# Optimization experiments

Measured on AMD Instinct MI355X. Metric: run time of the kernel, lower is better.

Reference implementation:

```python
import jax, jax.numpy as jnp
import numpy as np

NUM_STEPS = 3
NUM_HEADS = 8
HEAD_DIM = 128
EPS = 1e-5


def layernorm(x, g, b):
    mu = jnp.mean(x, -1, keepdims=True)
    var = jnp.mean(jnp.square(x - mu), -1, keepdims=True)
    return (x - mu) * jax.lax.rsqrt(var + EPS) * g + b


def entmax15(x):
    # Exact entmax-1.5 along last axis (Peters & Martins 2019, sort-based).
    x = (x - jnp.max(x, -1, keepdims=True)) / 2.0
    xs = jnp.flip(jnp.sort(x, -1), -1)  # descending sort
    rho = jnp.arange(1, x.shape[-1] + 1, dtype=x.dtype)
    mean = jnp.cumsum(xs, -1) / rho
    meansq = jnp.cumsum(xs * xs, -1) / rho
    ss = rho * (meansq - jnp.square(mean))
    tau = mean - jnp.sqrt(jnp.clip((1.0 - ss) / rho, 0.0, None))
    support = jnp.sum(tau <= xs, -1, keepdims=True)
    tau_star = jnp.take_along_axis(tau, support - 1, -1)
    return jnp.square(jnp.clip(x - tau_star, 0.0, None))


def setup_inputs() -> dict:
    key = jax.random.key(0)
    ks = jax.random.split(key, 6)
    B, S, Hd, Md, N = 2, 1024, 2048, 1024, 2048
    THD = NUM_HEADS * HEAD_DIM
    return {
        "hidden": jax.random.normal(ks[0], (B, S, Hd), jnp.float32),
        "memory": jax.random.normal(ks[1], (N, Md), jnp.float32),
        "Wq": jax.random.normal(ks[2], (THD, Hd), jnp.float32) / np.float32(np.sqrt(Hd)),
        "Wk": jax.random.normal(ks[3], (THD, Md), jnp.float32) / np.float32(np.sqrt(Md)),
        "Wv": jax.random.normal(ks[4], (THD, Md), jnp.float32) / np.float32(np.sqrt(Md)),
        "Wo": jax.random.normal(ks[5], (Hd, THD), jnp.float32) / np.float32(np.sqrt(THD)),
        "log_beta": jnp.full((NUM_HEADS,), float(np.log(1.0 / np.sqrt(HEAD_DIM))), jnp.float32),
        "g_state": jnp.ones((Hd,), jnp.float32),
        "b_state": jnp.zeros((Hd,), jnp.float32),
        "g_mem": jnp.ones((Md,), jnp.float32),
        "b_mem": jnp.zeros((Md,), jnp.float32),
    }


def reference(hidden, memory, Wq, Wk, Wv, Wo, log_beta, g_state, b_state, g_mem, b_mem):
    B, S, _ = hidden.shape
    N = memory.shape[0]
    H, hd = NUM_HEADS, HEAD_DIM
    # projections
    Q = layernorm(hidden, g_state, b_state) @ Wq.T            # (B,S,H*hd)
    mn = layernorm(memory, g_mem, b_mem)                      # (N,Md)
    K = (mn @ Wk.T).reshape(N, H, hd).transpose(1, 0, 2)      # (H,N,hd)
    V = (mn @ Wv.T).reshape(N, H, hd).transpose(1, 0, 2)      # (H,N,hd)
    xi = Q.reshape(B, S, H, hd).transpose(0, 2, 1, 3)          # (B,H,S,hd)
    beta = jnp.exp(log_beta)[None, :, None, None]
    for _ in range(NUM_STEPS):
        scores = jnp.einsum('bhsd,hnd->bhsn', xi, K) * beta    # (B,H,S,N)
        w = entmax15(scores)
        xi = jnp.einsum('bhsn,hnd->bhsd', w, V)
    out = xi.transpose(0, 2, 1, 3).reshape(B, S, H * hd) @ Wo.T  # (B,S,hidden_dim)
    return out
```

## Files before the change

### kernel.cpp

```cpp
#include <hip/hip_runtime.h>

typedef _Float16 half8 __attribute__((ext_vector_type(8)));
typedef _Float16 hv4 __attribute__((ext_vector_type(4)));
typedef float fv4 __attribute__((ext_vector_type(4)));

typedef __attribute__((address_space(3))) unsigned lds_u32;
typedef const __attribute__((address_space(1))) unsigned glb_u32;

__device__ __forceinline__ void gll16(const void* g, void* l) {
  __builtin_amdgcn_global_load_lds((glb_u32*)g, (lds_u32*)l, 16, 0, 0);
}

__device__ __forceinline__ void ln_body(const float* __restrict__ in, const float* __restrict__ g,
                                        const float* __restrict__ bb, _Float16* __restrict__ out,
                                        int ncols, int row) {
  __shared__ float sm[8];
  int t = threadIdx.x;
  const float* rp = in + (size_t)row * ncols;
  int nv = ncols >> 10;
  fv4 v[2];
  float s1 = 0.f, s2 = 0.f;
#pragma unroll
  for (int c = 0; c < 2; ++c)
    if (c < nv) {
      v[c] = *(const fv4*)(rp + c * 1024 + t * 4);
#pragma unroll
      for (int j = 0; j < 4; ++j) { s1 += v[c][j]; s2 += v[c][j] * v[c][j]; }
    }
#pragma unroll
  for (int off = 32; off > 0; off >>= 1) { s1 += __shfl_xor(s1, off, 64); s2 += __shfl_xor(s2, off, 64); }
  int w = t >> 6;
  if ((t & 63) == 0) { sm[w] = s1; sm[4 + w] = s2; }
  __syncthreads();
  s1 = sm[0] + sm[1] + sm[2] + sm[3];
  s2 = sm[4] + sm[5] + sm[6] + sm[7];
  float inv = 1.0f / (float)ncols;
  float mu = s1 * inv;
  float var = s2 * inv - mu * mu;
  float rstd = rsqrtf(var + 1e-5f);
#pragma unroll
  for (int c = 0; c < 2; ++c)
    if (c < nv) {
      int col = c * 1024 + t * 4;
      fv4 gg = *(const fv4*)(g + col);
      fv4 bv = *(const fv4*)(bb + col);
      hv4 o;
#pragma unroll
      for (int j = 0; j < 4; ++j) o[j] = (_Float16)(((v[c][j] - mu) * rstd) * gg[j] + bv[j]);
      *(hv4*)(out + (size_t)row * ncols + col) = o;
    }
}

__global__ __launch_bounds__(256) void ln_all(const float* __restrict__ hid,
                                              const float* __restrict__ mem,
                                              const float* __restrict__ gs, const float* __restrict__ bs,
                                              const float* __restrict__ gm, const float* __restrict__ bm,
                                              _Float16* __restrict__ oh, _Float16* __restrict__ om) {
  int b = blockIdx.x;
  if (b < 2048) ln_body(hid, gs, bs, oh, 2048, b);
  else ln_body(mem, gm, bm, om, 1024, b - 2048);
}

__global__ __launch_bounds__(256) void cast_all(const float* __restrict__ s0, _Float16* __restrict__ d0,
                                                const float* __restrict__ s1, _Float16* __restrict__ d1,
                                                const float* __restrict__ s2, _Float16* __restrict__ d2,
                                                const float* __restrict__ s3, _Float16* __restrict__ d3) {
  int b = blockIdx.x;
  const float* s;
  _Float16* d;
  int off;
  if (b < 2048) { s = s0; d = d0; off = b; }
  else if (b < 3072) { s = s1; d = d1; off = b - 2048; }
  else if (b < 4096) { s = s2; d = d2; off = b - 3072; }
  else { s = s3; d = d3; off = b - 4096; }
  int i = (off * 256 + threadIdx.x) << 2;
  fv4 f = *(const fv4*)(s + i);
  hv4 h;
#pragma unroll
  for (int j = 0; j < 4; ++j) h[j] = (_Float16)f[j];
  *(hv4*)(d + i) = h;
}

__global__ __launch_bounds__(256) void reduce_split(const float* __restrict__ parts, int ns,
                                                    long long stride,
                                                    _Float16* __restrict__ hi, int n) {
  int i = (blockIdx.x * 256 + threadIdx.x) << 2;
  if (i < n) {
    fv4 s = *(const fv4*)(parts + i);
    for (int j = 1; j < ns; ++j) {
      fv4 v = *(const fv4*)(parts + (size_t)j * stride + i);
      s += v;
    }
    hv4 h;
#pragma unroll
    for (int j = 0; j < 4; ++j) h[j] = (_Float16)s[j];
    *(hv4*)(hi + i) = h;
  }
}

__global__ __launch_bounds__(256) void entmax_c(const _Float16* __restrict__ scores,
                                                float* __restrict__ crow) {
  __shared__ float comp[4][512];
  int wid = threadIdx.x >> 6;
  int row = blockIdx.x * 4 + wid;
  int l = threadIdx.x & 63;
  unsigned long long lmask = (1ull << l) - 1ull;
  const half8* sp = (const half8*)(scores + (size_t)row * 2048);
  half8 hx[4];
#pragma unroll
  for (int i = 0; i < 4; ++i) hx[i] = sp[i * 64 + l];
  fv4 x[8];
#pragma unroll
  for (int i = 0; i < 4; ++i)
#pragma unroll
    for (int j = 0; j < 8; ++j) x[i * 2 + (j >> 2)][j & 3] = (float)hx[i][j];
  float m = x[0][0];
#pragma unroll
  for (int i = 0; i < 8; ++i)
#pragma unroll
    for (int j = 0; j < 4; ++j) m = fmaxf(m, x[i][j]);
#pragma unroll
  for (int off = 32; off > 0; off >>= 1) m = fmaxf(m, __shfl_xor(m, off, 64));
#pragma unroll
  for (int i = 0; i < 8; ++i)
#pragma unroll
    for (int j = 0; j < 4; ++j) x[i][j] = (x[i][j] - m) * 0.5f;

  float tau = -1.0f;
  bool fixed = false;
  int cnti = 2048;
  for (int it = 0; it < 6 && !fixed; ++it) {
    float s1 = 0.f, s2 = 0.f;
    cnti = 0;
#pragma unroll
    for (int i = 0; i < 8; ++i)
#pragma unroll
      for (int j = 0; j < 4; ++j) {
        bool a = x[i][j] > tau;
        cnti += (int)__builtin_popcountll(__ballot(a));
        float sel = a ? x[i][j] : 0.f;
        s1 += sel;
        s2 = fmaf(sel, sel, s2);
      }
#pragma unroll
    for (int off = 32; off > 0; off >>= 1) {
      s1 += __shfl_xor(s1, off, 64);
      s2 += __shfl_xor(s2, off, 64);
    }
    float cnt = (float)cnti;
    float mean = s1 / cnt;
    float ss = s2 - s1 * mean;
    float nt = mean - sqrtf(fmaxf((1.0f - ss) / cnt, 0.0f));
    if (nt == tau) fixed = true;
    else tau = nt;
    if (cnti <= 512) break;
  }
  if (!fixed) {
    if (cnti <= 512) {
      int base = 0;
#pragma unroll
      for (int i = 0; i < 8; ++i)
#pragma unroll
        for (int j = 0; j < 4; ++j) {
          bool a = x[i][j] > tau;
          unsigned long long mk = __ballot(a);
          if (a) comp[wid][base + (int)__builtin_popcountll(mk & lmask)] = x[i][j];
          base += (int)__builtin_popcountll(mk);
        }
      float y[8];
#pragma unroll
      for (int r = 0; r < 8; ++r) {
        int idx = r * 64 + l;
        y[r] = (idx < base) ? comp[wid][idx] : -2.0f;
      }
      for (int it = 0; it < 10 && !fixed; ++it) {
        float s1 = 0.f, s2 = 0.f;
        int c = 0;
#pragma unroll
        for (int r = 0; r < 8; ++r) {
          bool a = y[r] > tau;
          c += (int)__builtin_popcountll(__ballot(a));
          float sel = a ? y[r] : 0.f;
          s1 += sel;
          s2 = fmaf(sel, sel, s2);
        }
#pragma unroll
        for (int off = 32; off > 0; off >>= 1) {
          s1 += __shfl_xor(s1, off, 64);
          s2 += __shfl_xor(s2, off, 64);
        }
        float cnt = (float)c;
        float mean = s1 / cnt;
        float ss = s2 - s1 * mean;
        float nt = mean - sqrtf(fmaxf((1.0f - ss) / cnt, 0.0f));
        if (nt == tau) fixed = true;
        else tau = nt;
      }
    } else {
      for (int it = 0; it < 8 && !fixed; ++it) {
        float s1 = 0.f, s2 = 0.f;
        int c = 0;
#pragma unroll
        for (int i = 0; i < 8; ++i)
#pragma unroll
          for (int j = 0; j < 4; ++j) {
            bool a = x[i][j] > tau;
            c += (int)__builtin_popcountll(__ballot(a));
            float sel = a ? x[i][j] : 0.f;
            s1 += sel;
            s2 = fmaf(sel, sel, s2);
          }
#pragma unroll
        for (int off = 32; off > 0; off >>= 1) {
          s1 += __shfl_xor(s1, off, 64);
          s2 += __shfl_xor(s2, off, 64);
        }
        float cnt = (float)c;
        float mean = s1 / cnt;
        float ss = s2 - s1 * mean;
        float nt = mean - sqrtf(fmaxf((1.0f - ss) / cnt, 0.0f));
        if (nt == tau) fixed = true;
        else tau = nt;
      }
    }
  }

  if (l == 0) crow[row] = 0.5f * m + tau;
}

struct GemmParams {
  const _Float16 *A, *B, *B2;
  const float* crow;
  _Float16 *C16, *C16b;
  float* C32;
  const float* log_beta;
  int K, lda, ldb;
  long long aSB, aSH, bSH;
  long long crowSB, crowSH;
  long long cSB, cSH, cOsR, cOsC;
  long long cOsRb, cOsCb;
  long long partStride;
  int alphaMode, outMode, outModeB, nsplit, dual;
  int gx, gy, swz;
};

template <int AMODE>
__device__ __forceinline__ void gemm_body(const GemmParams& p, int bx, int by, int bz) {
  __shared__ __align__(16) _Float16 As[3][128 * 32];
  __shared__ __align__(16) _Float16 Bs[3][128 * 32];
  int t = threadIdx.x;
  int m0 = by * 128;
  int n0, kbeg, kend, ks = 0;
  if (p.nsplit > 1) {
    ks = bx % p.nsplit;
    n0 = (bx / p.nsplit) * 128;
    int kl = p.K / p.nsplit;
    kbeg = ks * kl;
    kend = kbeg + kl;
  } else {
    n0 = bx * 128;
    kbeg = 0;
    kend = p.K;
  }
  int bidx, h, job = 0;
  if (p.dual) { job = bz; bidx = 0; h = 0; }
  else { bidx = bz >> 3; h = bz & 7; }
  const _Float16* pA = p.A + bidx * p.aSB + h * p.aSH;
  const _Float16* pB = (job ? p.B2 : p.B) + h * p.bSH;

  fv4 acc[4][4] = {};
  int wv = t >> 6, l = t & 63, quad = l >> 4, lr = l & 15;
  int wm = (wv >> 1) * 64, wn = (wv & 1) * 64;
  int rl = l >> 2;
  int cs = (((l & 3) ^ ((l >> 3) & 3)) << 3);
  int rsw = (lr >> 1) & 3;

  float cr[4];
  if (AMODE == 1) {
    const float* pc = p.crow + bidx * p.crowSB + h * p.crowSH;
#pragma unroll
    for (int mi = 0; mi < 4; ++mi) cr[mi] = pc[m0 + wm + mi * 16 + lr];
    asm volatile("s_waitcnt vmcnt(0)" ::: "memory");
  }

  auto STAGE = [&](int buf, int k0) {
#pragma unroll
    for (int v = 0; v < 2; ++v) {
      int rb = wv * 16 + v * 64;
      int r = rb + rl;
      gll16(pA + (size_t)(m0 + r) * p.lda + k0 + cs, &As[buf][rb * 32]);
      gll16(pB + (size_t)(n0 + r) * p.ldb + k0 + cs, &Bs[buf][rb * 32]);
    }
  };

  int nk = (kend - kbeg) >> 5;
  STAGE(0, kbeg);
  if (nk > 1) STAGE(1, kbeg + 32);
  int cur = 0;
  for (int ti = 0; ti < nk; ++ti) {
    if (ti + 1 < nk) asm volatile("s_waitcnt vmcnt(4)" ::: "memory");
    else asm volatile("s_waitcnt vmcnt(0)" ::: "memory");
    __builtin_amdgcn_s_barrier();
    __builtin_amdgcn_sched_barrier(0);
    if (ti + 2 < nk) {
      int nb = cur + 2;
      if (nb >= 3) nb -= 3;
      STAGE(nb, kbeg + ((ti + 2) << 5));
    }
    __builtin_amdgcn_sched_barrier(0);
    half8 ah[4], bh[4];
#pragma unroll
    for (int mi = 0; mi < 4; ++mi) {
      half8 a = *(const half8*)&As[cur][(wm + mi * 16 + lr) * 32 + ((quad ^ rsw) << 3)];
      if (AMODE == 1) {
        half8 d = a * (_Float16)0.5f - (_Float16)cr[mi];
        d = __builtin_elementwise_max(d, (half8)(0));
        a = d * d;
      }
      ah[mi] = a;
    }
#pragma unroll
    for (int ni = 0; ni < 4; ++ni)
      bh[ni] = *(const half8*)&Bs[cur][(wn + ni * 16 + lr) * 32 + ((quad ^ rsw) << 3)];
    __builtin_amdgcn_s_setprio(1);
#pragma unroll
    for (int mi = 0; mi < 4; ++mi)
#pragma unroll
      for (int ni = 0; ni < 4; ++ni)
        acc[mi][ni] = __builtin_amdgcn_mfma_f32_16x16x32_f16(ah[mi], bh[ni], acc[mi][ni], 0, 0, 0);
    __builtin_amdgcn_s_setprio(0);
    cur = (cur == 2) ? 0 : cur + 1;
  }

  float alpha = p.alphaMode ? __expf(p.log_beta[h]) : 1.0f;
  int om = (p.dual && job) ? p.outModeB : p.outMode;
  _Float16* c16 = (p.dual && job) ? p.C16b : p.C16;
  long long osR = (p.dual && job) ? p.cOsRb : p.cOsR;
  long long osC = (p.dual && job) ? p.cOsCb : p.cOsC;
  float* c32 = p.C32 + (p.nsplit > 1 ? (long long)ks * p.partStride : 0);
  long long cOff = (long long)bidx * p.cSB + (long long)h * p.cSH;
#pragma unroll
  for (int mi = 0; mi < 4; ++mi)
#pragma unroll
    for (int ni = 0; ni < 4; ++ni) {
      int row = m0 + wm + mi * 16 + quad * 4;
      int col = n0 + wn + ni * 16 + lr;
#pragma unroll
      for (int r = 0; r < 4; ++r) {
        float val = acc[mi][ni][r] * alpha;
        long long idx = cOff + (long long)(row + r) * osR + (long long)col * osC;
        if (om == 1) c32[idx] = val;
        else c16[idx] = (_Float16)val;
      }
    }
}

template <int AMODE>
__global__ __launch_bounds__(256) void gemm_nt(GemmParams p) {
  int id = blockIdx.x;
  if (p.swz) {
    int q = (int)gridDim.x >> 3;
    id = (id & 7) * q + (id >> 3);
  }
  int bx = id % p.gx;
  int r = id / p.gx;
  gemm_body<AMODE>(p, bx, r % p.gy, r / p.gy);
}

__global__ __launch_bounds__(256) void gemm_pair(GemmParams a, GemmParams b, int na) {
  int id = blockIdx.x;
  if (id < na) {
    int bx = id % a.gx;
    int r = id / a.gx;
    gemm_body<0>(a, bx, r % a.gy, r / a.gy);
  } else {
    int j = id - na;
    int bx = j % b.gx;
    int r = j / b.gx;
    gemm_body<0>(b, bx, r % b.gy, r / b.gy);
  }
}

extern "C" void kernel_launch(void* const* d_in, const int* in_sizes, int n_in,
                              void* d_out, int out_size, void* d_ws, size_t ws_size,
                              hipStream_t stream) {
  const float* hidden = (const float*)d_in[0];
  const float* memory = (const float*)d_in[1];
  const float* Wq = (const float*)d_in[2];
  const float* Wk = (const float*)d_in[3];
  const float* Wv = (const float*)d_in[4];
  const float* Wo = (const float*)d_in[5];
  const float* log_beta = (const float*)d_in[6];
  const float* g_state = (const float*)d_in[7];
  const float* b_state = (const float*)d_in[8];
  const float* g_mem = (const float*)d_in[9];
  const float* b_mem = (const float*)d_in[10];

  char* w = (char*)d_ws;
  auto alloc = [&](size_t bytes) {
    char* r = w;
    w += (bytes + 255) & ~(size_t)255;
    return r;
  };
  _Float16* wq16 = (_Float16*)alloc(2097152 * 2);
  _Float16* wk16 = (_Float16*)alloc(1048576 * 2);
  _Float16* wv16 = (_Float16*)alloc(1048576 * 2);
  _Float16* wo16 = (_Float16*)alloc(2097152 * 2);
  _Float16* lnh16 = (_Float16*)alloc(4194304 * 2);
  _Float16* mn16 = (_Float16*)alloc(2097152 * 2);
  _Float16* kph = (_Float16*)alloc(2097152 * 2);
  _Float16* vt16 = (_Float16*)alloc(2097152 * 2);
  _Float16* xih = (_Float16*)alloc(2097152 * 2);
  float* parts = (float*)alloc((size_t)8 * 2097152 * 4);
  _Float16* scores16 = (_Float16*)alloc((size_t)33554432 * 2);
  float* crow = (float*)alloc(16384 * 4);

  ln_all<<<4096, 256, 0, stream>>>(hidden, memory, g_state, b_state, g_mem, b_mem, lnh16, mn16);
  cast_all<<<6144, 256, 0, stream>>>(Wq, wq16, Wk, wk16, Wv, wv16, Wo, wo16);

  {
    GemmParams pq{};
    pq.A = lnh16; pq.lda = 2048;
    pq.B = wq16; pq.ldb = 2048;
    pq.K = 2048; pq.nsplit = 2;
    pq.C32 = parts; pq.outMode = 1; pq.partStride = 2097152;
    pq.cOsR = 1024; pq.cOsC = 1;
    pq.gx = 16; pq.gy = 16;

    GemmParams pkv{};
    pkv.A = mn16; pkv.lda = 1024;
    pkv.B = wk16; pkv.B2 = wv16; pkv.ldb = 1024;
    pkv.K = 1024; pkv.dual = 1;
    pkv.C16 = kph; pkv.outMode = 0; pkv.cOsR = 1024; pkv.cOsC = 1;
    pkv.C16b = vt16; pkv.outModeB = 0; pkv.cOsRb = 1; pkv.cOsCb = 2048;
    pkv.gx = 8; pkv.gy = 16;

    gemm_pair<<<512, 256, 0, stream>>>(pq, pkv, 256);
    reduce_split<<<2048, 256, 0, stream>>>(parts, 2, 2097152, xih, 2097152);
  }

  for (int step = 0; step < 3; ++step) {
    {
      GemmParams p{};
      p.A = xih;
      p.lda = 1024; p.aSB = 1048576; p.aSH = 128;
      p.B = kph; p.ldb = 1024; p.bSH = 128;
      p.K = 128;
      p.alphaMode = 1; p.log_beta = log_beta;
      p.C16 = scores16; p.outMode = 0;
      p.cSB = 16777216; p.cSH = 2097152;
      p.cOsR = 2048; p.cOsC = 1;
      p.gx = 16; p.gy = 8; p.swz = 1;
      gemm_nt<0><<<2048, 256, 0, stream>>>(p);
    }
    entmax_c<<<4096, 256, 0, stream>>>(scores16, crow);
    {
      GemmParams p{};
      p.A = scores16; p.crow = crow;
      p.lda = 2048; p.aSB = 16777216; p.aSH = 2097152;
      p.crowSB = 8192; p.crowSH = 1024;
      p.B = vt16; p.ldb = 2048; p.bSH = 262144;
      p.K = 2048; p.nsplit = 4;
      p.C32 = parts; p.outMode = 1; p.partStride = 2097152;
      p.cSB = 1048576; p.cSH = 128;
      p.cOsR = 1024; p.cOsC = 1;
      p.gx = 4; p.gy = 8; p.swz = 1;
      gemm_nt<1><<<512, 256, 0, stream>>>(p);
    }
    reduce_split<<<2048, 256, 0, stream>>>(parts, 4, 2097152, xih, 2097152);
  }

  {
    GemmParams p{};
    p.A = xih; p.lda = 1024;
    p.B = wo16; p.ldb = 1024;
    p.K = 1024;
    p.C32 = (float*)d_out; p.outMode = 1;
    p.cOsR = 2048; p.cOsC = 1;
    p.gx = 16; p.gy = 16; p.swz = 1;
    gemm_nt<0><<<256, 256, 0, stream>>>(p);
  }
}
```

Measured before the change: 424.2 us.

## Fuse score GEMM, entmax threshold and weighted-V GEMM into one step kernel

Each Hopfield step was four kernels: a scores GEMM, an entmax threshold kernel, a split-K W·V GEMM and a split reduction. They are replaced by a single kernel in which each block owns 16 query rows of one head. The block computes the full 2048-wide score row in MFMA registers, finds the entmax threshold by fixed-point iteration with block-level reductions, writes the squared weights to swizzled LDS, and multiplies them against V straight into the output. This removes the large fp16 score buffer round trip and several launches per step. In exchange, every block re-reads the whole K and V of its head from global or L2 with a small row tile, the LDS footprint is large, and each threshold iteration needs a __syncthreads.

```diff
diff --git a/kernel.cpp b/kernel.cpp
--- a/kernel.cpp
+++ b/kernel.cpp
@@ -98,153 +98,169 @@
   }
 }
 
-__global__ __launch_bounds__(256) void entmax_c(const _Float16* __restrict__ scores,
-                                                float* __restrict__ crow) {
-  __shared__ float comp[4][512];
-  int wid = threadIdx.x >> 6;
-  int row = blockIdx.x * 4 + wid;
-  int l = threadIdx.x & 63;
-  unsigned long long lmask = (1ull << l) - 1ull;
-  const half8* sp = (const half8*)(scores + (size_t)row * 2048);
-  half8 hx[4];
-#pragma unroll
-  for (int i = 0; i < 4; ++i) hx[i] = sp[i * 64 + l];
-  fv4 x[8];
-#pragma unroll
-  for (int i = 0; i < 4; ++i)
-#pragma unroll
-    for (int j = 0; j < 8; ++j) x[i * 2 + (j >> 2)][j & 3] = (float)hx[i][j];
-  float m = x[0][0];
-#pragma unroll
-  for (int i = 0; i < 8; ++i)
-#pragma unroll
-    for (int j = 0; j < 4; ++j) m = fmaxf(m, x[i][j]);
-#pragma unroll
-  for (int off = 32; off > 0; off >>= 1) m = fmaxf(m, __shfl_xor(m, off, 64));
-#pragma unroll
-  for (int i = 0; i < 8; ++i)
-#pragma unroll
-    for (int j = 0; j < 4; ++j) x[i][j] = (x[i][j] - m) * 0.5f;
+__global__ __launch_bounds__(256) void fused_step(const _Float16* __restrict__ xi,
+                                                  const _Float16* __restrict__ kp,
+                                                  const _Float16* __restrict__ vt,
+                                                  const float* __restrict__ log_beta,
+                                                  _Float16* __restrict__ xo) {
+  __shared__ __align__(16) _Float16 wlds[16 * 2048];
+  float* red = (float*)wlds;
+
+  int t = threadIdx.x;
+  int wv = t >> 6, l = t & 63;
+  int lr = l & 15, quad = l >> 4;
+
+  int id = blockIdx.x;
+  int h = id & 7;
+  int rbb = id >> 3;
+  int b = rbb >> 6;
+  int r0 = (rbb & 63) << 4;
+
+  const _Float16* xiP = xi + ((size_t)(b * 1024 + r0)) * 1024 + h * 128;
+  const _Float16* kP = kp + (size_t)h * 128;
+  int sbase = wv * 512;
+
+  half8 bx[4];
+#pragma unroll
+  for (int c = 0; c < 4; ++c)
+    bx[c] = *(const half8*)(xiP + (size_t)lr * 1024 + c * 32 + quad * 8);
+
+  fv4 sc[32];
+  half8 ka[2][4];
+#pragma unroll
+  for (int c = 0; c < 4; ++c)
+    ka[0][c] = *(const half8*)(kP + (size_t)(sbase + lr) * 1024 + c * 32 + quad * 8);
+#pragma unroll
+  for (int f = 0; f < 32; ++f) {
+    const int cu = f & 1;
+    if (f + 1 < 32) {
+      int slot = sbase + (f + 1) * 16 + lr;
+#pragma unroll
+      for (int c = 0; c < 4; ++c)
+        ka[cu ^ 1][c] = *(const half8*)(kP + (size_t)slot * 1024 + c * 32 + quad * 8);
+    }
+    fv4 a = {0.f, 0.f, 0.f, 0.f};
+#pragma unroll
+    for (int c = 0; c < 4; ++c)
+      a = __builtin_amdgcn_mfma_f32_16x16x32_f16(ka[cu][c], bx[c], a, 0, 0, 0);
+    sc[f] = a;
+  }
+
+  float m = sc[0][0];
+#pragma unroll
+  for (int f = 0; f < 32; ++f)
+#pragma unroll
+    for (int r = 0; r < 4; ++r) m = fmaxf(m, sc[f][r]);
+  m = fmaxf(m, __shfl_xor(m, 16, 64));
+  m = fmaxf(m, __shfl_xor(m, 32, 64));
+  if (l < 16) red[wv * 48 + l] = m;
+  __syncthreads();
+  m = fmaxf(fmaxf(red[lr], red[48 + lr]), fmaxf(red[96 + lr], red[144 + lr]));
+
+  float a05 = 0.5f * __expf(log_beta[h]);
+  float nc = -a05 * m;
+#pragma unroll
+  for (int f = 0; f < 32; ++f)
+#pragma unroll
+    for (int r = 0; r < 4; ++r) sc[f][r] = fmaf(a05, sc[f][r], nc);
 
   float tau = -1.0f;
-  bool fixed = false;
-  int cnti = 2048;
-  for (int it = 0; it < 6 && !fixed; ++it) {
-    float s1 = 0.f, s2 = 0.f;
-    cnti = 0;
-#pragma unroll
-    for (int i = 0; i < 8; ++i)
-#pragma unroll
-      for (int j = 0; j < 4; ++j) {
-        bool a = x[i][j] > tau;
-        cnti += (int)__builtin_popcountll(__ballot(a));
-        float sel = a ? x[i][j] : 0.f;
+  int par = 1;
+#pragma unroll 1
+  for (int it = 0; it < 20; ++it) {
+    float cf = 0.f, s1 = 0.f, s2 = 0.f;
+#pragma unroll
+    for (int f = 0; f < 32; ++f)
+#pragma unroll
+      for (int r = 0; r < 4; ++r) {
+        float v = sc[f][r];
+        bool pb = v > tau;
+        float sel = pb ? v : 0.f;
+        cf += pb ? 1.f : 0.f;
         s1 += sel;
         s2 = fmaf(sel, sel, s2);
       }
-#pragma unroll
-    for (int off = 32; off > 0; off >>= 1) {
-      s1 += __shfl_xor(s1, off, 64);
-      s2 += __shfl_xor(s2, off, 64);
-    }
-    float cnt = (float)cnti;
-    float mean = s1 / cnt;
-    float ss = s2 - s1 * mean;
-    float nt = mean - sqrtf(fmaxf((1.0f - ss) / cnt, 0.0f));
-    if (nt == tau) fixed = true;
-    else tau = nt;
-    if (cnti <= 512) break;
-  }
-  if (!fixed) {
-    if (cnti <= 512) {
-      int base = 0;
-#pragma unroll
-      for (int i = 0; i < 8; ++i)
-#pragma unroll
-        for (int j = 0; j < 4; ++j) {
-          bool a = x[i][j] > tau;
-          unsigned long long mk = __ballot(a);
-          if (a) comp[wid][base + (int)__builtin_popcountll(mk & lmask)] = x[i][j];
-          base += (int)__builtin_popcountll(mk);
-        }
-      float y[8];
-#pragma unroll
-      for (int r = 0; r < 8; ++r) {
-        int idx = r * 64 + l;
-        y[r] = (idx < base) ? comp[wid][idx] : -2.0f;
+    cf += __shfl_xor(cf, 16, 64); cf += __shfl_xor(cf, 32, 64);
+    s1 += __shfl_xor(s1, 16, 64); s1 += __shfl_xor(s1, 32, 64);
+    s2 += __shfl_xor(s2, 16, 64); s2 += __shfl_xor(s2, 32, 64);
+    float* wr = red + par * 192 + wv * 48;
+    if (l < 16) { wr[l] = cf; wr[16 + l] = s1; wr[32 + l] = s2; }
+    __syncthreads();
+    float C = 0.f, S1 = 0.f, S2 = 0.f;
+#pragma unroll
+    for (int w2 = 0; w2 < 4; ++w2) {
+      const float* rr = red + par * 192 + w2 * 48;
+      C += rr[lr]; S1 += rr[16 + lr]; S2 += rr[32 + lr];
+    }
+    par ^= 1;
+    float mean = S1 / C;
+    float ssv = S2 - S1 * mean;
+    float nt = mean - sqrtf(fmaxf((1.0f - ssv) / C, 0.0f));
+    bool conv = (nt == tau);
+    tau = nt;
+    if (__all(conv)) break;
+  }
+  __syncthreads();
+
+  unsigned swz = (unsigned)((lr & 7) << 4);
+#pragma unroll
+  for (int f = 0; f < 32; ++f) {
+    hv4 hw;
+#pragma unroll
+    for (int r = 0; r < 4; ++r) {
+      float d = fmaxf(sc[f][r] - tau, 0.f);
+      hw[r] = (_Float16)(d * d);
+    }
+    unsigned byteoff = ((unsigned)lr * 4096) + (((unsigned)((sbase + f * 16 + quad * 4) * 2)) ^ swz);
+    *(hv4*)((char*)wlds + byteoff) = hw;
+  }
+  __syncthreads();
+
+  const _Float16* vP = vt + ((size_t)(h * 128 + wv * 32)) * 2048;
+  fv4 o0[2] = {}, o1[2] = {};
+#pragma unroll 2
+  for (int kt = 0; kt < 64; kt += 2) {
+    {
+      unsigned ab = (unsigned)lr * 4096 + (((unsigned)((kt * 32 + quad * 8) * 2)) ^ swz);
+      half8 aw = *(const half8*)((char*)wlds + ab);
+#pragma unroll
+      for (int ni = 0; ni < 2; ++ni) {
+        half8 bv = *(const half8*)(vP + (size_t)(ni * 16 + lr) * 2048 + kt * 32 + quad * 8);
+        o0[ni] = __builtin_amdgcn_mfma_f32_16x16x32_f16(aw, bv, o0[ni], 0, 0, 0);
       }
-      for (int it = 0; it < 10 && !fixed; ++it) {
-        float s1 = 0.f, s2 = 0.f;
-        int c = 0;
-#pragma unroll
-        for (int r = 0; r < 8; ++r) {
-          bool a = y[r] > tau;
-          c += (int)__builtin_popcountll(__ballot(a));
-          float sel = a ? y[r] : 0.f;
-          s1 += sel;
-          s2 = fmaf(sel, sel, s2);
-        }
-#pragma unroll
-        for (int off = 32; off > 0; off >>= 1) {
-          s1 += __shfl_xor(s1, off, 64);
-          s2 += __shfl_xor(s2, off, 64);
-        }
-        float cnt = (float)c;
-        float mean = s1 / cnt;
-        float ss = s2 - s1 * mean;
-        float nt = mean - sqrtf(fmaxf((1.0f - ss) / cnt, 0.0f));
-        if (nt == tau) fixed = true;
-        else tau = nt;
+    }
+    {
+      unsigned ab = (unsigned)lr * 4096 + (((unsigned)(((kt + 1) * 32 + quad * 8) * 2)) ^ swz);
+      half8 aw = *(const half8*)((char*)wlds + ab);
+#pragma unroll
+      for (int ni = 0; ni < 2; ++ni) {
+        half8 bv = *(const half8*)(vP + (size_t)(ni * 16 + lr) * 2048 + (kt + 1) * 32 + quad * 8);
+        o1[ni] = __builtin_amdgcn_mfma_f32_16x16x32_f16(aw, bv, o1[ni], 0, 0, 0);
       }
-    } else {
-      for (int it = 0; it < 8 && !fixed; ++it) {
-        float s1 = 0.f, s2 = 0.f;
-        int c = 0;
-#pragma unroll
-        for (int i = 0; i < 8; ++i)
-#pragma unroll
-          for (int j = 0; j < 4; ++j) {
-            bool a = x[i][j] > tau;
-            c += (int)__builtin_popcountll(__ballot(a));
-            float sel = a ? x[i][j] : 0.f;
-            s1 += sel;
-            s2 = fmaf(sel, sel, s2);
-          }
-#pragma unroll
-        for (int off = 32; off > 0; off >>= 1) {
-          s1 += __shfl_xor(s1, off, 64);
-          s2 += __shfl_xor(s2, off, 64);
-        }
-        float cnt = (float)c;
-        float mean = s1 / cnt;
-        float ss = s2 - s1 * mean;
-        float nt = mean - sqrtf(fmaxf((1.0f - ss) / cnt, 0.0f));
-        if (nt == tau) fixed = true;
-        else tau = nt;
-      }
-    }
-  }
-
-  if (l == 0) crow[row] = 0.5f * m + tau;
+    }
+  }
+
+  _Float16* op = xo + ((size_t)(b * 1024 + r0)) * 1024 + h * 128 + wv * 32;
+#pragma unroll
+  for (int ni = 0; ni < 2; ++ni)
+#pragma unroll
+    for (int r = 0; r < 4; ++r)
+      op[(size_t)(quad * 4 + r) * 1024 + ni * 16 + lr] = (_Float16)(o0[ni][r] + o1[ni][r]);
 }
 
 struct GemmParams {
   const _Float16 *A, *B, *B2;
-  const float* crow;
   _Float16 *C16, *C16b;
   float* C32;
-  const float* log_beta;
   int K, lda, ldb;
   long long aSB, aSH, bSH;
-  long long crowSB, crowSH;
   long long cSB, cSH, cOsR, cOsC;
   long long cOsRb, cOsCb;
   long long partStride;
-  int alphaMode, outMode, outModeB, nsplit, dual;
+  int outMode, outModeB, nsplit, dual;
   int gx, gy, swz;
 };
 
-template <int AMODE>
 __device__ __forceinline__ void gemm_body(const GemmParams& p, int bx, int by, int bz) {
   __shared__ __align__(16) _Float16 As[3][128 * 32];
   __shared__ __align__(16) _Float16 Bs[3][128 * 32];
@@ -275,14 +291,6 @@
   int cs = (((l & 3) ^ ((l >> 3) & 3)) << 3);
   int rsw = (lr >> 1) & 3;
 
-  float cr[4];
-  if (AMODE == 1) {
-    const float* pc = p.crow + bidx * p.crowSB + h * p.crowSH;
-#pragma unroll
-    for (int mi = 0; mi < 4; ++mi) cr[mi] = pc[m0 + wm + mi * 16 + lr];
-    asm volatile("s_waitcnt vmcnt(0)" ::: "memory");
-  }
-
   auto STAGE = [&](int buf, int k0) {
 #pragma unroll
     for (int v = 0; v < 2; ++v) {
@@ -310,15 +318,8 @@
     __builtin_amdgcn_sched_barrier(0);
     half8 ah[4], bh[4];
 #pragma unroll
-    for (int mi = 0; mi < 4; ++mi) {
-      half8 a = *(const half8*)&As[cur][(wm + mi * 16 + lr) * 32 + ((quad ^ rsw) << 3)];
-      if (AMODE == 1) {
-        half8 d = a * (_Float16)0.5f - (_Float16)cr[mi];
-        d = __builtin_elementwise_max(d, (half8)(0));
-        a = d * d;
-      }
-      ah[mi] = a;
-    }
+    for (int mi = 0; mi < 4; ++mi)
+      ah[mi] = *(const half8*)&As[cur][(wm + mi * 16 + lr) * 32 + ((quad ^ rsw) << 3)];
 #pragma unroll
     for (int ni = 0; ni < 4; ++ni)
       bh[ni] = *(const half8*)&Bs[cur][(wn + ni * 16 + lr) * 32 + ((quad ^ rsw) << 3)];
@@ -332,7 +333,6 @@
     cur = (cur == 2) ? 0 : cur + 1;
   }
 
-  float alpha = p.alphaMode ? __expf(p.log_beta[h]) : 1.0f;
   int om = (p.dual && job) ? p.outModeB : p.outMode;
   _Float16* c16 = (p.dual && job) ? p.C16b : p.C16;
   long long osR = (p.dual && job) ? p.cOsRb : p.cOsR;
@@ -347,7 +347,7 @@
       int col = n0 + wn + ni * 16 + lr;
 #pragma unroll
       for (int r = 0; r < 4; ++r) {
-        float val = acc[mi][ni][r] * alpha;
+        float val = acc[mi][ni][r];
         long long idx = cOff + (long long)(row + r) * osR + (long long)col * osC;
         if (om == 1) c32[idx] = val;
         else c16[idx] = (_Float16)val;
@@ -355,7 +355,6 @@
     }
 }
 
-template <int AMODE>
 __global__ __launch_bounds__(256) void gemm_nt(GemmParams p) {
   int id = blockIdx.x;
   if (p.swz) {
@@ -364,7 +363,7 @@
   }
   int bx = id % p.gx;
   int r = id / p.gx;
-  gemm_body<AMODE>(p, bx, r % p.gy, r / p.gy);
+  gemm_body(p, bx, r % p.gy, r / p.gy);
 }
 
 __global__ __launch_bounds__(256) void gemm_pair(GemmParams a, GemmParams b, int na) {
@@ -372,12 +371,12 @@
   if (id < na) {
     int bx = id % a.gx;
     int r = id / a.gx;
-    gemm_body<0>(a, bx, r % a.gy, r / a.gy);
+    gemm_body(a, bx, r % a.gy, r / a.gy);
   } else {
     int j = id - na;
     int bx = j % b.gx;
     int r = j / b.gx;
-    gemm_body<0>(b, bx, r % b.gy, r / b.gy);
+    gemm_body(b, bx, r % b.gy, r / b.gy);
   }
 }
 
@@ -411,9 +410,7 @@
   _Float16* kph = (_Float16*)alloc(2097152 * 2);
   _Float16* vt16 = (_Float16*)alloc(2097152 * 2);
   _Float16* xih = (_Float16*)alloc(2097152 * 2);
-  float* parts = (float*)alloc((size_t)8 * 2097152 * 4);
-  _Float16* scores16 = (_Float16*)alloc((size_t)33554432 * 2);
-  float* crow = (float*)alloc(16384 * 4);
+  float* parts = (float*)alloc((size_t)2 * 2097152 * 4);
 
   ln_all<<<4096, 256, 0, stream>>>(hidden, memory, g_state, b_state, g_mem, b_mem, lnh16, mn16);
   cast_all<<<6144, 256, 0, stream>>>(Wq, wq16, Wk, wk16, Wv, wv16, Wo, wo16);
@@ -439,36 +436,8 @@
     reduce_split<<<2048, 256, 0, stream>>>(parts, 2, 2097152, xih, 2097152);
   }
 
-  for (int step = 0; step < 3; ++step) {
-    {
-      GemmParams p{};
-      p.A = xih;
-      p.lda = 1024; p.aSB = 1048576; p.aSH = 128;
-      p.B = kph; p.ldb = 1024; p.bSH = 128;
-      p.K = 128;
-      p.alphaMode = 1; p.log_beta = log_beta;
-      p.C16 = scores16; p.outMode = 0;
-      p.cSB = 16777216; p.cSH = 2097152;
-      p.cOsR = 2048; p.cOsC = 1;
-      p.gx = 16; p.gy = 8; p.swz = 1;
-      gemm_nt<0><<<2048, 256, 0, stream>>>(p);
-    }
-    entmax_c<<<4096, 256, 0, stream>>>(scores16, crow);
-    {
-      GemmParams p{};
-      p.A = scores16; p.crow = crow;
-      p.lda = 2048; p.aSB = 16777216; p.aSH = 2097152;
-      p.crowSB = 8192; p.crowSH = 1024;
-      p.B = vt16; p.ldb = 2048; p.bSH = 262144;
-      p.K = 2048; p.nsplit = 4;
-      p.C32 = parts; p.outMode = 1; p.partStride = 2097152;
-      p.cSB = 1048576; p.cSH = 128;
-      p.cOsR = 1024; p.cOsC = 1;
-      p.gx = 4; p.gy = 8; p.swz = 1;
-      gemm_nt<1><<<512, 256, 0, stream>>>(p);
-    }
-    reduce_split<<<2048, 256, 0, stream>>>(parts, 4, 2097152, xih, 2097152);
-  }
+  for (int step = 0; step < 3; ++step)
+    fused_step<<<1024, 256, 0, stream>>>(xih, kph, vt16, log_beta, xih);
 
   {
     GemmParams p{};
@@ -478,6 +447,6 @@
     p.C32 = (float*)d_out; p.outMode = 1;
     p.cOsR = 2048; p.cOsC = 1;
     p.gx = 16; p.gy = 16; p.swz = 1;
-    gemm_nt<0><<<256, 256, 0, stream>>>(p);
-  }
-}
+    gemm_nt<<<256, 256, 0, stream>>>(p);
+  }
+}
```

Result: slower. 704.7 us (+66.1%).
